# Kernel tuning notes

Measured on AMD Instinct MI355X. Metric: run time of the kernel, lower is better.

Reference implementation:

```python
import jax, jax.numpy as jnp
import numpy as np

B = 8192
IN = 512          # inputs feature dim (input_size[2])
CTX = 256         # context_input_size
CENTER = 512      # center_size
MIN_ = IN + CTX   # module_input_size = 768
FF = 1024         # n_ff_pre_units
RNN = 1024        # n_rnn_units
OUT = 512         # output_size
O2C = 256         # output_to_center_size
TOT = OUT + O2C   # total_output_size = 768


def setup_inputs() -> dict:
    key = jax.random.key(0)
    ks = jax.random.split(key, 12)
    return {
        "inputs": jax.random.normal(ks[0], (B, 1, IN), jnp.float32),
        "center_state": jax.random.normal(ks[1], (B, 1, CENTER), jnp.float32),
        "module_state": jax.random.normal(ks[2], (B, 1, RNN), jnp.float32),
        # reading_weights: truncated normal stddev 0.1 in TF; plain normal*0.1 is fine for a math reference
        "W_read": jax.random.normal(ks[3], (CENTER, CTX), jnp.float32) * 0.1,
        "W_pre": jax.random.normal(ks[4], (MIN_, FF), jnp.float32) * (1.0 / np.sqrt(MIN_)),
        "b_pre": jnp.zeros((FF,), jnp.float32),
        "Wx": jax.random.normal(ks[5], (FF, RNN), jnp.float32) * (1.0 / np.sqrt(FF)),
        "Wh": jax.random.normal(ks[6], (RNN, RNN), jnp.float32) * (1.0 / np.sqrt(RNN)),
        "b_rnn": jnp.zeros((RNN,), jnp.float32),
        "W_post": jax.random.normal(ks[7], (RNN, TOT), jnp.float32) * (1.0 / np.sqrt(RNN)),
        "b_post": jnp.zeros((TOT,), jnp.float32),
    }


def reference(inputs, center_state, module_state, W_read, W_pre, b_pre, Wx, Wh, b_rnn, W_post, b_post):
    # tf.clip_by_norm(W, 1.0): global Frobenius norm clip
    norm = jnp.sqrt(jnp.sum(W_read * W_read))
    W_clip = W_read * (1.0 / jnp.maximum(norm, 1.0))
    # context read: [B,1,CENTER] @ [CENTER,CTX] -> [B,1,CTX]
    context = jnp.einsum("btc,cd->btd", center_state, W_clip)
    module_inputs = jnp.concatenate([inputs, context], axis=2)  # [B,1,MIN_]
    rnn_in = jax.nn.relu(jnp.einsum("btf,fg->btg", module_inputs, W_pre) + b_pre)
    # SimpleRNNCell: h' = tanh(x Wx + h Wh + b)
    h_new = jnp.tanh(jnp.einsum("btf,fg->btg", rnn_in, Wx)
                     + jnp.einsum("btf,fg->btg", module_state, Wh) + b_rnn)
    module_output = jax.nn.relu(jnp.einsum("btf,fg->btg", h_new, W_post) + b_post)
    network_output = module_output[:, :, :OUT]
    module_output_to_center = module_output[:, :, OUT:]
    return (network_output, module_output_to_center, h_new)
```

## Files before the change

### kernel.cpp

```cpp
#include <hip/hip_runtime.h>

typedef __bf16 bf16x8 __attribute__((ext_vector_type(8)));
typedef float  f32x4  __attribute__((ext_vector_type(4)));
typedef unsigned short ushort8 __attribute__((ext_vector_type(8)));

#define B_ROWS 8192
#define IN_D   512
#define CTX_D  256
#define CENTER 512
#define MIN_D  768
#define FF_D   1024
#define RNN_D  1024
#define OUT_D  512
#define O2C_D  256
#define TOT_D  768

__device__ __forceinline__ unsigned short f2bf(float f) {
    unsigned int u = __builtin_bit_cast(unsigned int, f);
    u = (u + 0x7fff + ((u >> 16) & 1)) >> 16;
    return (unsigned short)u;
}

__device__ __forceinline__ void load_lds16(const void* g, void* l) {
    __builtin_amdgcn_global_load_lds(
        (const __attribute__((address_space(1))) unsigned int*)g,
        (__attribute__((address_space(3))) unsigned int*)l, 16, 0, 0);
}

__launch_bounds__(256)
__global__ void reduce_sq(const float* __restrict__ w, float* __restrict__ ss, int n) {
    float s = 0.f;
    for (int i = blockIdx.x * blockDim.x + threadIdx.x; i < n; i += gridDim.x * blockDim.x) {
        float v = w[i]; s += v * v;
    }
    #pragma unroll
    for (int off = 32; off > 0; off >>= 1) s += __shfl_down(s, off, 64);
    if ((threadIdx.x & 63) == 0) atomicAdd(ss, s);
}

__launch_bounds__(256)
__global__ void cvt_w_all(const float* __restrict__ Wpre, const float* __restrict__ Wx,
                          const float* __restrict__ Wh,  const float* __restrict__ Wpost,
                          const float* __restrict__ Wread,
                          unsigned short* __restrict__ WpreT, unsigned short* __restrict__ WxhT,
                          unsigned short* __restrict__ WpostT, unsigned short* __restrict__ WreadT) {
    int g = blockIdx.x * 256 + threadIdx.x;
    const float* W; unsigned short* out; int N, ostride;
    if (g < 98304)        { W = Wpre;  out = WpreT;        N = 1024; ostride = 768;  }
    else if (g < 229376)  { g -= 98304;  W = Wx;   out = WxhT;        N = 1024; ostride = 2048; }
    else if (g < 360448)  { g -= 229376; W = Wh;   out = WxhT + 1024; N = 1024; ostride = 2048; }
    else if (g < 458752)  { g -= 360448; W = Wpost; out = WpostT;     N = 768;  ostride = 1024; }
    else                  { g -= 458752; W = Wread; out = WreadT;     N = 256;  ostride = 512;  }
    int n  = g % N;
    int kg = g / N;
    ushort8 o;
    #pragma unroll
    for (int j = 0; j < 8; ++j)
        o[j] = f2bf(W[(long)(kg * 8 + j) * N + n]);
    *(ushort8*)(out + (long)n * ostride + kg * 8) = o;
}

__launch_bounds__(256)
__global__ void cvt_act_all(const float* __restrict__ center, const float* __restrict__ inputs,
                            const float* __restrict__ mstate,
                            unsigned short* __restrict__ csB, unsigned short* __restrict__ miB,
                            unsigned short* __restrict__ rnB) {
    long g = (long)blockIdx.x * 256 + threadIdx.x;
    const float* src; unsigned short* dst; int logc, ostride;
    if (g < 524288)       { src = center; dst = csB;        logc = 9;  ostride = 512;  }
    else if (g < 1048576) { g -= 524288;  src = inputs; dst = miB;        logc = 9;  ostride = 768;  }
    else                  { g -= 1048576; src = mstate; dst = rnB + 1024; logc = 10; ostride = 2048; }
    long e = g * 8;
    long row = e >> logc;
    int  col = (int)(e & ((1 << logc) - 1));
    f32x4 v0 = *(const f32x4*)(src + e);
    f32x4 v1 = *(const f32x4*)(src + e + 4);
    ushort8 o;
    o[0] = f2bf(v0[0]); o[1] = f2bf(v0[1]); o[2] = f2bf(v0[2]); o[3] = f2bf(v0[3]);
    o[4] = f2bf(v1[0]); o[5] = f2bf(v1[1]); o[6] = f2bf(v1[2]); o[7] = f2bf(v1[3]);
    *(ushort8*)(dst + row * (long)ostride + col) = o;
}

template<int MODE>
__launch_bounds__(256, 4)
__global__ void gemm_bt(const unsigned short* __restrict__ A,
                        const unsigned short* __restrict__ Bt,
                        int K, const float* __restrict__ bias,
                        unsigned short* __restrict__ outB, int ldob,
                        float* __restrict__ outF, int ldof) {
    __shared__ alignas(16) unsigned short sA[128 * 64];
    __shared__ alignas(16) unsigned short sB[64 * 64];

    const int tid  = threadIdx.x;
    const int wave = tid >> 6;
    const int lane = tid & 63;
    const int bm = blockIdx.x, bn = blockIdx.y;
    const int wm = wave & 1, wn = wave >> 1;
    const int lr = lane >> 4;
    const int lc = lane & 15;
    const int sw = lc & 7;

    f32x4 acc[4][2] = {};

    long aoff[4], boff[2];
    #pragma unroll
    for (int j = 0; j < 4; ++j) {
        const int c   = tid + j * 256;
        const int row = c >> 3;
        const int kg  = (c & 7) ^ (row & 7);
        aoff[j] = (long)(bm * 128 + row) * K + kg * 8;
    }
    #pragma unroll
    for (int j = 0; j < 2; ++j) {
        const int c   = tid + j * 256;
        const int row = c >> 3;
        const int kg  = (c & 7) ^ (row & 7);
        boff[j] = (long)(bn * 64 + row) * K + kg * 8;
    }

    for (int k0 = 0; k0 < K; k0 += 64) {
        #pragma unroll
        for (int j = 0; j < 4; ++j)
            load_lds16(A + aoff[j] + k0, (char*)sA + j * 4096 + wave * 1024);
        #pragma unroll
        for (int j = 0; j < 2; ++j)
            load_lds16(Bt + boff[j] + k0, (char*)sB + j * 4096 + wave * 1024);
        __syncthreads();

        #pragma unroll
        for (int kh = 0; kh < 2; ++kh) {
            const int ch = (kh * 4 + lr) ^ sw;
            bf16x8 af[4], bfr[2];
            #pragma unroll
            for (int t = 0; t < 4; ++t)
                af[t] = *(const bf16x8*)(sA + (wm * 64 + t * 16 + lc) * 64 + ch * 8);
            #pragma unroll
            for (int u = 0; u < 2; ++u)
                bfr[u] = *(const bf16x8*)(sB + (wn * 32 + u * 16 + lc) * 64 + ch * 8);
            #pragma unroll
            for (int i = 0; i < 4; ++i)
                #pragma unroll
                for (int u = 0; u < 2; ++u)
                    acc[i][u] = __builtin_amdgcn_mfma_f32_16x16x32_bf16(af[i], bfr[u], acc[i][u], 0, 0, 0);
        }
        __syncthreads();
    }

    float sc = 1.f;
    if constexpr (MODE == 0) sc = 1.f / fmaxf(sqrtf(*bias), 1.f);
    #pragma unroll
    for (int u = 0; u < 2; ++u) {
        const int gcol = bn * 64 + wn * 32 + u * 16 + lc;
        float bv = 0.f;
        if constexpr (MODE != 0) bv = bias[gcol];
        #pragma unroll
        for (int tm = 0; tm < 4; ++tm) {
            const int grow0 = bm * 128 + wm * 64 + tm * 16 + lr * 4;
            #pragma unroll
            for (int r = 0; r < 4; ++r) {
                const long grow = grow0 + r;
                float v = acc[tm][u][r];
                if constexpr (MODE == 0) v *= sc;
                else v += bv;
                if constexpr (MODE == 1 || MODE == 3) v = fmaxf(v, 0.f);
                if constexpr (MODE == 2) v = tanhf(v);
                if constexpr (MODE == 0 || MODE == 1 || MODE == 2)
                    outB[grow * (long)ldob + gcol] = f2bf(v);
                if constexpr (MODE == 2)
                    outF[grow * (long)ldof + gcol] = v;
                if constexpr (MODE == 3) {
                    if (gcol < OUT_D)
                        outF[grow * OUT_D + gcol] = v;
                    else
                        outF[(long)B_ROWS * OUT_D + grow * O2C_D + (gcol - OUT_D)] = v;
                }
            }
        }
    }
}

extern "C" void kernel_launch(void* const* d_in, const int* in_sizes, int n_in,
                              void* d_out, int out_size, void* d_ws, size_t ws_size,
                              hipStream_t stream) {
    const float* inputs = (const float*)d_in[0];
    const float* center = (const float*)d_in[1];
    const float* mstate = (const float*)d_in[2];
    const float* W_read = (const float*)d_in[3];
    const float* W_pre  = (const float*)d_in[4];
    const float* b_pre  = (const float*)d_in[5];
    const float* Wx     = (const float*)d_in[6];
    const float* Wh     = (const float*)d_in[7];
    const float* b_rnn  = (const float*)d_in[8];
    const float* W_post = (const float*)d_in[9];
    const float* b_post = (const float*)d_in[10];
    float* out = (float*)d_out;

    char* ws = (char*)d_ws;
    float* ss = (float*)ws;
    unsigned short* WreadT = (unsigned short*)(ws + 256);
    unsigned short* WpreT  = WreadT + 256 * 512;
    unsigned short* WxhT   = WpreT  + 1024 * 768;
    unsigned short* WpostT = WxhT   + (long)1024 * 2048;
    unsigned short* csB    = WpostT + 768 * 1024;
    unsigned short* miB    = csB + (long)B_ROWS * CENTER;
    unsigned short* rnB    = miB + (long)B_ROWS * MIN_D;
    unsigned short* hB     = rnB + (long)B_ROWS * 2048;

    hipMemsetAsync(ss, 0, 4, stream);
    reduce_sq<<<128, 256, 0, stream>>>(W_read, ss, CENTER * CTX_D);

    cvt_w_all<<<1856, 256, 0, stream>>>(W_pre, Wx, Wh, W_post, W_read,
                                        WpreT, WxhT, WpostT, WreadT);
    cvt_act_all<<<8192, 256, 0, stream>>>(center, inputs, mstate, csB, miB, rnB);

    gemm_bt<0><<<dim3(64, 4), 256, 0, stream>>>(csB, WreadT, 512, ss,
                                                miB + 512, MIN_D, nullptr, 0);
    gemm_bt<1><<<dim3(64, 16), 256, 0, stream>>>(miB, WpreT, 768, b_pre,
                                                 rnB, 2048, nullptr, 0);
    gemm_bt<2><<<dim3(64, 16), 256, 0, stream>>>(rnB, WxhT, 2048, b_rnn,
                                                 hB, RNN_D,
                                                 out + (long)B_ROWS * TOT_D, RNN_D);
    gemm_bt<3><<<dim3(64, 12), 256, 0, stream>>>(hB, WpostT, 1024, b_post,
                                                 nullptr, 0, out, 0);
}
```

Baseline: 255.6 us.

## Double-buffer LDS tiles in bf16 GEMM with manual vmcnt waits

Gives the GEMM kernel two LDS buffers for the A and B tiles. The global-to-LDS loads for the next K-step are issued while the current tile is being computed, using raw s_barrier plus explicit vmcnt waits in place of __syncthreads, so memory latency can overlap with MFMA work. The doubled LDS footprint lowers the occupancy target from 4 to 3 blocks per CU. The hand-coded waitcnt values and the two-step loop assume an even number of K tiles and exactly six outstanding loads per stage.

```diff
diff --git a/kernel.cpp b/kernel.cpp
--- a/kernel.cpp
+++ b/kernel.cpp
@@ -26,6 +26,10 @@
         (const __attribute__((address_space(1))) unsigned int*)g,
         (__attribute__((address_space(3))) unsigned int*)l, 16, 0, 0);
 }
+
+#define RAW_BARRIER() asm volatile("s_barrier" : : : "memory")
+#define WAIT_VM6() __builtin_amdgcn_s_waitcnt(0x0F76)
+#define WAIT_VM0() __builtin_amdgcn_s_waitcnt(0x0F70)
 
 __launch_bounds__(256)
 __global__ void reduce_sq(const float* __restrict__ w, float* __restrict__ ss, int n) {
@@ -82,14 +86,16 @@
 }
 
 template<int MODE>
-__launch_bounds__(256, 4)
+__launch_bounds__(256, 3)
 __global__ void gemm_bt(const unsigned short* __restrict__ A,
                         const unsigned short* __restrict__ Bt,
                         int K, const float* __restrict__ bias,
                         unsigned short* __restrict__ outB, int ldob,
                         float* __restrict__ outF, int ldof) {
-    __shared__ alignas(16) unsigned short sA[128 * 64];
-    __shared__ alignas(16) unsigned short sB[64 * 64];
+    __shared__ alignas(16) unsigned short sA0[128 * 64];
+    __shared__ alignas(16) unsigned short sB0[64 * 64];
+    __shared__ alignas(16) unsigned short sA1[128 * 64];
+    __shared__ alignas(16) unsigned short sB1[64 * 64];
 
     const int tid  = threadIdx.x;
     const int wave = tid >> 6;
@@ -118,33 +124,56 @@
         boff[j] = (long)(bn * 64 + row) * K + kg * 8;
     }
 
-    for (int k0 = 0; k0 < K; k0 += 64) {
+    auto issue = [&](int k0, unsigned short* dA, unsigned short* dB) {
         #pragma unroll
         for (int j = 0; j < 4; ++j)
-            load_lds16(A + aoff[j] + k0, (char*)sA + j * 4096 + wave * 1024);
+            load_lds16(A + aoff[j] + k0, (char*)dA + j * 4096 + wave * 1024);
         #pragma unroll
         for (int j = 0; j < 2; ++j)
-            load_lds16(Bt + boff[j] + k0, (char*)sB + j * 4096 + wave * 1024);
-        __syncthreads();
-
+            load_lds16(Bt + boff[j] + k0, (char*)dB + j * 4096 + wave * 1024);
+    };
+    auto compute = [&](const unsigned short* cA, const unsigned short* cB) {
         #pragma unroll
         for (int kh = 0; kh < 2; ++kh) {
             const int ch = (kh * 4 + lr) ^ sw;
             bf16x8 af[4], bfr[2];
             #pragma unroll
             for (int t = 0; t < 4; ++t)
-                af[t] = *(const bf16x8*)(sA + (wm * 64 + t * 16 + lc) * 64 + ch * 8);
+                af[t] = *(const bf16x8*)(cA + (wm * 64 + t * 16 + lc) * 64 + ch * 8);
             #pragma unroll
             for (int u = 0; u < 2; ++u)
-                bfr[u] = *(const bf16x8*)(sB + (wn * 32 + u * 16 + lc) * 64 + ch * 8);
+                bfr[u] = *(const bf16x8*)(cB + (wn * 32 + u * 16 + lc) * 64 + ch * 8);
             #pragma unroll
             for (int i = 0; i < 4; ++i)
                 #pragma unroll
                 for (int u = 0; u < 2; ++u)
                     acc[i][u] = __builtin_amdgcn_mfma_f32_16x16x32_bf16(af[i], bfr[u], acc[i][u], 0, 0, 0);
         }
-        __syncthreads();
-    }
+    };
+
+    const int NK = K >> 6;
+    issue(0,  sA0, sB0);
+    issue(64, sA1, sB1);
+
+    for (int k = 0; k + 2 < NK; k += 2) {
+        WAIT_VM6();
+        RAW_BARRIER();
+        compute(sA0, sB0);
+        RAW_BARRIER();
+        issue((k + 2) * 64, sA0, sB0);
+        WAIT_VM6();
+        RAW_BARRIER();
+        compute(sA1, sB1);
+        RAW_BARRIER();
+        if (k + 3 < NK) issue((k + 3) * 64, sA1, sB1);
+    }
+    WAIT_VM6();
+    RAW_BARRIER();
+    compute(sA0, sB0);
+    RAW_BARRIER();
+    WAIT_VM0();
+    RAW_BARRIER();
+    compute(sA1, sB1);
 
     float sc = 1.f;
     if constexpr (MODE == 0) sc = 1.f / fmaxf(sqrtf(*bias), 1.f);
```

Result: slower. 263.5 us (+3.1%).

## Merge prep kernels into one launch and use 128x128 GEMM tiles with BK=32

Applied to the files above, without the earlier changes.

Three preprocessing kernels plus the memset are merged into a single prep_all launch. The norm reduction now writes per-block partials that the first GEMM sums itself, which removes the atomic and the memset. The GEMM tile grows from 128x64 to 128x128 (4x4 MFMA accumulators per wave) with K-step 32, a new LDS swizzle, and a swapped grid order so N-blocks of the same M row run adjacently. This raises arithmetic intensity and cuts launch overhead, but doubles the accumulator registers (launch bounds drop to 2) and halves the K work per barrier.

```diff
diff --git a/kernel.cpp b/kernel.cpp
--- a/kernel.cpp
+++ b/kernel.cpp
@@ -28,44 +28,47 @@
 }
 
 __launch_bounds__(256)
-__global__ void reduce_sq(const float* __restrict__ w, float* __restrict__ ss, int n) {
-    float s = 0.f;
-    for (int i = blockIdx.x * blockDim.x + threadIdx.x; i < n; i += gridDim.x * blockDim.x) {
-        float v = w[i]; s += v * v;
-    }
-    #pragma unroll
-    for (int off = 32; off > 0; off >>= 1) s += __shfl_down(s, off, 64);
-    if ((threadIdx.x & 63) == 0) atomicAdd(ss, s);
-}
-
-__launch_bounds__(256)
-__global__ void cvt_w_all(const float* __restrict__ Wpre, const float* __restrict__ Wx,
-                          const float* __restrict__ Wh,  const float* __restrict__ Wpost,
-                          const float* __restrict__ Wread,
-                          unsigned short* __restrict__ WpreT, unsigned short* __restrict__ WxhT,
-                          unsigned short* __restrict__ WpostT, unsigned short* __restrict__ WreadT) {
-    int g = blockIdx.x * 256 + threadIdx.x;
-    const float* W; unsigned short* out; int N, ostride;
-    if (g < 98304)        { W = Wpre;  out = WpreT;        N = 1024; ostride = 768;  }
-    else if (g < 229376)  { g -= 98304;  W = Wx;   out = WxhT;        N = 1024; ostride = 2048; }
-    else if (g < 360448)  { g -= 229376; W = Wh;   out = WxhT + 1024; N = 1024; ostride = 2048; }
-    else if (g < 458752)  { g -= 360448; W = Wpost; out = WpostT;     N = 768;  ostride = 1024; }
-    else                  { g -= 458752; W = Wread; out = WreadT;     N = 256;  ostride = 512;  }
-    int n  = g % N;
-    int kg = g / N;
-    ushort8 o;
-    #pragma unroll
-    for (int j = 0; j < 8; ++j)
-        o[j] = f2bf(W[(long)(kg * 8 + j) * N + n]);
-    *(ushort8*)(out + (long)n * ostride + kg * 8) = o;
-}
-
-__launch_bounds__(256)
-__global__ void cvt_act_all(const float* __restrict__ center, const float* __restrict__ inputs,
-                            const float* __restrict__ mstate,
-                            unsigned short* __restrict__ csB, unsigned short* __restrict__ miB,
-                            unsigned short* __restrict__ rnB) {
-    long g = (long)blockIdx.x * 256 + threadIdx.x;
+__global__ void prep_all(const float* __restrict__ Wread, float* __restrict__ partials,
+                         const float* __restrict__ Wpre, const float* __restrict__ Wx,
+                         const float* __restrict__ Wh,  const float* __restrict__ Wpost,
+                         unsigned short* __restrict__ WpreT, unsigned short* __restrict__ WxhT,
+                         unsigned short* __restrict__ WpostT, unsigned short* __restrict__ WreadT,
+                         const float* __restrict__ center, const float* __restrict__ inputs,
+                         const float* __restrict__ mstate,
+                         unsigned short* __restrict__ csB, unsigned short* __restrict__ miB,
+                         unsigned short* __restrict__ rnB) {
+    const int bid = blockIdx.x;
+    const int tid = threadIdx.x;
+    if (bid < 128) {
+        __shared__ float red[4];
+        const float* p = Wread + bid * 1024 + tid * 4;
+        f32x4 v = *(const f32x4*)p;
+        float s = v[0]*v[0] + v[1]*v[1] + v[2]*v[2] + v[3]*v[3];
+        #pragma unroll
+        for (int off = 32; off > 0; off >>= 1) s += __shfl_down(s, off, 64);
+        if ((tid & 63) == 0) red[tid >> 6] = s;
+        __syncthreads();
+        if (tid == 0) partials[bid] = red[0] + red[1] + red[2] + red[3];
+        return;
+    }
+    if (bid < 1984) {
+        int g = (bid - 128) * 256 + tid;
+        const float* W; unsigned short* out; int N, ostride;
+        if (g < 98304)        { W = Wpre;  out = WpreT;        N = 1024; ostride = 768;  }
+        else if (g < 229376)  { g -= 98304;  W = Wx;    out = WxhT;        N = 1024; ostride = 2048; }
+        else if (g < 360448)  { g -= 229376; W = Wh;    out = WxhT + 1024; N = 1024; ostride = 2048; }
+        else if (g < 458752)  { g -= 360448; W = Wpost; out = WpostT;      N = 768;  ostride = 1024; }
+        else                  { g -= 458752; W = Wread; out = WreadT;      N = 256;  ostride = 512;  }
+        int n  = g % N;
+        int kg = g / N;
+        ushort8 o;
+        #pragma unroll
+        for (int j = 0; j < 8; ++j)
+            o[j] = f2bf(W[(long)(kg * 8 + j) * N + n]);
+        *(ushort8*)(out + (long)n * ostride + kg * 8) = o;
+        return;
+    }
+    long g = (long)(bid - 1984) * 256 + tid;
     const float* src; unsigned short* dst; int logc, ostride;
     if (g < 524288)       { src = center; dst = csB;        logc = 9;  ostride = 512;  }
     else if (g < 1048576) { g -= 524288;  src = inputs; dst = miB;        logc = 9;  ostride = 768;  }
@@ -82,75 +85,70 @@
 }
 
 template<int MODE>
-__launch_bounds__(256, 4)
+__launch_bounds__(256, 2)
 __global__ void gemm_bt(const unsigned short* __restrict__ A,
                         const unsigned short* __restrict__ Bt,
                         int K, const float* __restrict__ bias,
                         unsigned short* __restrict__ outB, int ldob,
                         float* __restrict__ outF, int ldof) {
-    __shared__ alignas(16) unsigned short sA[128 * 64];
-    __shared__ alignas(16) unsigned short sB[64 * 64];
+    __shared__ alignas(16) unsigned short sA[128 * 32];
+    __shared__ alignas(16) unsigned short sB[128 * 32];
 
     const int tid  = threadIdx.x;
     const int wave = tid >> 6;
     const int lane = tid & 63;
-    const int bm = blockIdx.x, bn = blockIdx.y;
+    const int bn = blockIdx.x, bm = blockIdx.y;
     const int wm = wave & 1, wn = wave >> 1;
     const int lr = lane >> 4;
     const int lc = lane & 15;
-    const int sw = lc & 7;
-
-    f32x4 acc[4][2] = {};
-
-    long aoff[4], boff[2];
-    #pragma unroll
-    for (int j = 0; j < 4; ++j) {
-        const int c   = tid + j * 256;
-        const int row = c >> 3;
-        const int kg  = (c & 7) ^ (row & 7);
-        aoff[j] = (long)(bm * 128 + row) * K + kg * 8;
-    }
+
+    f32x4 acc[4][4] = {};
+
+    long aoff[2], boff[2];
     #pragma unroll
     for (int j = 0; j < 2; ++j) {
         const int c   = tid + j * 256;
-        const int row = c >> 3;
-        const int kg  = (c & 7) ^ (row & 7);
-        boff[j] = (long)(bn * 64 + row) * K + kg * 8;
-    }
-
-    for (int k0 = 0; k0 < K; k0 += 64) {
-        #pragma unroll
-        for (int j = 0; j < 4; ++j)
-            load_lds16(A + aoff[j] + k0, (char*)sA + j * 4096 + wave * 1024);
-        #pragma unroll
-        for (int j = 0; j < 2; ++j)
+        const int row = c >> 2;
+        const int kg  = (c & 3) ^ (row & 3);
+        aoff[j] = (long)(bm * 128 + row) * K + kg * 8;
+        boff[j] = (long)(bn * 128 + row) * K + kg * 8;
+    }
+
+    const int rsw = lr ^ (lc & 3);
+
+    for (int k0 = 0; k0 < K; k0 += 32) {
+        #pragma unroll
+        for (int j = 0; j < 2; ++j) {
+            load_lds16(A  + aoff[j] + k0, (char*)sA + j * 4096 + wave * 1024);
             load_lds16(Bt + boff[j] + k0, (char*)sB + j * 4096 + wave * 1024);
-        __syncthreads();
-
-        #pragma unroll
-        for (int kh = 0; kh < 2; ++kh) {
-            const int ch = (kh * 4 + lr) ^ sw;
-            bf16x8 af[4], bfr[2];
-            #pragma unroll
-            for (int t = 0; t < 4; ++t)
-                af[t] = *(const bf16x8*)(sA + (wm * 64 + t * 16 + lc) * 64 + ch * 8);
-            #pragma unroll
-            for (int u = 0; u < 2; ++u)
-                bfr[u] = *(const bf16x8*)(sB + (wn * 32 + u * 16 + lc) * 64 + ch * 8);
-            #pragma unroll
-            for (int i = 0; i < 4; ++i)
-                #pragma unroll
-                for (int u = 0; u < 2; ++u)
-                    acc[i][u] = __builtin_amdgcn_mfma_f32_16x16x32_bf16(af[i], bfr[u], acc[i][u], 0, 0, 0);
         }
         __syncthreads();
+
+        bf16x8 af[4], bfr[4];
+        #pragma unroll
+        for (int t = 0; t < 4; ++t) {
+            const int ar = wm * 64 + t * 16 + lc;
+            af[t]  = *(const bf16x8*)(sA + ar * 32 + ((lr ^ (ar & 3)) * 8));
+            const int br = wn * 64 + t * 16 + lc;
+            bfr[t] = *(const bf16x8*)(sB + br * 32 + ((lr ^ (br & 3)) * 8));
+        }
+        #pragma unroll
+        for (int i = 0; i < 4; ++i)
+            #pragma unroll
+            for (int j2 = 0; j2 < 4; ++j2)
+                acc[i][j2] = __builtin_amdgcn_mfma_f32_16x16x32_bf16(af[i], bfr[j2], acc[i][j2], 0, 0, 0);
+        __syncthreads();
     }
 
     float sc = 1.f;
-    if constexpr (MODE == 0) sc = 1.f / fmaxf(sqrtf(*bias), 1.f);
+    if constexpr (MODE == 0) {
+        float s = 0.f;
+        for (int i = 0; i < 128; ++i) s += bias[i];
+        sc = 1.f / fmaxf(sqrtf(s), 1.f);
+    }
     #pragma unroll
-    for (int u = 0; u < 2; ++u) {
-        const int gcol = bn * 64 + wn * 32 + u * 16 + lc;
+    for (int tn = 0; tn < 4; ++tn) {
+        const int gcol = bn * 128 + wn * 64 + tn * 16 + lc;
         float bv = 0.f;
         if constexpr (MODE != 0) bv = bias[gcol];
         #pragma unroll
@@ -159,7 +157,7 @@
             #pragma unroll
             for (int r = 0; r < 4; ++r) {
                 const long grow = grow0 + r;
-                float v = acc[tm][u][r];
+                float v = acc[tm][tn][r];
                 if constexpr (MODE == 0) v *= sc;
                 else v += bv;
                 if constexpr (MODE == 1 || MODE == 3) v = fmaxf(v, 0.f);
@@ -196,8 +194,8 @@
     float* out = (float*)d_out;
 
     char* ws = (char*)d_ws;
-    float* ss = (float*)ws;
-    unsigned short* WreadT = (unsigned short*)(ws + 256);
+    float* partials = (float*)ws;
+    unsigned short* WreadT = (unsigned short*)(ws + 1024);
     unsigned short* WpreT  = WreadT + 256 * 512;
     unsigned short* WxhT   = WpreT  + 1024 * 768;
     unsigned short* WpostT = WxhT   + (long)1024 * 2048;
@@ -206,20 +204,18 @@
     unsigned short* rnB    = miB + (long)B_ROWS * MIN_D;
     unsigned short* hB     = rnB + (long)B_ROWS * 2048;
 
-    hipMemsetAsync(ss, 0, 4, stream);
-    reduce_sq<<<128, 256, 0, stream>>>(W_read, ss, CENTER * CTX_D);
-
-    cvt_w_all<<<1856, 256, 0, stream>>>(W_pre, Wx, Wh, W_post, W_read,
-                                        WpreT, WxhT, WpostT, WreadT);
-    cvt_act_all<<<8192, 256, 0, stream>>>(center, inputs, mstate, csB, miB, rnB);
-
-    gemm_bt<0><<<dim3(64, 4), 256, 0, stream>>>(csB, WreadT, 512, ss,
+    prep_all<<<10176, 256, 0, stream>>>(W_read, partials,
+                                        W_pre, Wx, Wh, W_post,
+                                        WpreT, WxhT, WpostT, WreadT,
+                                        center, inputs, mstate, csB, miB, rnB);
+
+    gemm_bt<0><<<dim3(2, 64), 256, 0, stream>>>(csB, WreadT, 512, partials,
                                                 miB + 512, MIN_D, nullptr, 0);
-    gemm_bt<1><<<dim3(64, 16), 256, 0, stream>>>(miB, WpreT, 768, b_pre,
-                                                 rnB, 2048, nullptr, 0);
-    gemm_bt<2><<<dim3(64, 16), 256, 0, stream>>>(rnB, WxhT, 2048, b_rnn,
-                                                 hB, RNN_D,
-                                                 out + (long)B_ROWS * TOT_D, RNN_D);
-    gemm_bt<3><<<dim3(64, 12), 256, 0, stream>>>(hB, WpostT, 1024, b_post,
-                                                 nullptr, 0, out, 0);
-}
+    gemm_bt<1><<<dim3(8, 64), 256, 0, stream>>>(miB, WpreT, 768, b_pre,
+                                                rnB, 2048, nullptr, 0);
+    gemm_bt<2><<<dim3(8, 64), 256, 0, stream>>>(rnB, WxhT, 2048, b_rnn,
+                                                hB, RNN_D,
+                                                out + (long)B_ROWS * TOT_D, RNN_D);
+    gemm_bt<3><<<dim3(6, 64), 256, 0, stream>>>(hB, WpostT, 1024, b_post,
+                                                nullptr, 0, out, 0);
+}
```

Measured after the change: 274.3 us. 7.3% more time.
